# Kernel optimization log

Measured on AMD Instinct MI355X. Metric: run time of the kernel, lower is better.

## Reference

```python
import jax, jax.numpy as jnp
import numpy as np

# ---- static config (from init_kwargs) ----
SAMPLE_RATE = 2048.0
MAX_SHIFT = int(0.025 * SAMPLE_RATE)          # 51 samples
NUM_BINS = 16
FFTLENGTH = 1.0                               # chisq_kernel_length (s)
DF = 1.0 / FFTLENGTH
NUM_FREQS = int(FFTLENGTH * SAMPLE_RATE // 2 + 1)   # 1025 == rfft bins of 2048 samples
HIGHPASS = 32.0
CHISQ_PENALTY = 1.0
_freqs = np.arange(NUM_FREQS) / FFTLENGTH
MASK = _freqs >= HIGHPASS                     # static numpy bool mask

BATCH, CHANNELS, DIM = 256, 2, 2048


def setup_inputs() -> dict:
    key = jax.random.key(0)
    k1, k2 = jax.random.split(key)
    x_hat = jax.random.normal(k1, (BATCH, CHANNELS, DIM), dtype=jnp.float32)
    x = jax.random.normal(k2, (BATCH, CHANNELS, DIM), dtype=jnp.float32)
    return {"x_hat": x_hat, "x": x}


def _center(x):
    xmin = x.min(-1, keepdims=True)
    xmax = x.max(-1, keepdims=True)
    return 2 * (x - xmin) / (xmax - xmin) - 1


def _shifted_pearson(x, y, max_shift):
    # x, y: [B, C, T]; returns corr: [W, B, C] with W = 2*max_shift + 1
    b, c, t = x.shape
    num_windows = 2 * max_shift + 1
    xp = jnp.pad(x, ((0, 0), (0, 0), (max_shift, max_shift)))
    # window w, position i -> xp[..., i + w]  (same layout as torch unfold)
    idx = jnp.arange(num_windows)[:, None] + jnp.arange(t)[None, :]   # [W, T]
    xw = xp[:, :, idx]                                                # [B, C, W, T]
    xw = jnp.transpose(xw, (2, 0, 1, 3))                              # [W, B, C, T]
    xw = xw - xw.mean(-1, keepdims=True)
    yc = y - y.mean(-1, keepdims=True)
    corr = (xw * yc).sum(-1)
    norm = (xw ** 2).sum(-1) * (yc ** 2).sum(-1)
    return corr / jnp.sqrt(norm)


def _snr_integral(a, b):
    # |4 * a * conj(b) * df| cumulatively summed over frequency
    integrand = a * jnp.conj(b)
    return jnp.abs(4 * integrand * DF).cumsum(-1)


def _chisq(htilde, stilde):
    htilde = htilde[:, :, MASK]
    stilde = stilde[:, :, MASK]
    # partition frequencies by the template's own optimal-SNR integral
    si = _snr_integral(htilde, htilde)                    # [B, C, F]
    total = si[:, :, -1:]
    bins = (jnp.arange(NUM_BINS + 1, dtype=si.dtype) / NUM_BINS) * total  # [B, C, NB+1]
    search = jax.vmap(jax.vmap(lambda a, v: jnp.searchsorted(a, v, side="right")))
    edges = search(si, bins)
    edges = jnp.clip(edges, 0, si.shape[-1] - 1)
    qtilde = htilde / jnp.sqrt(total).astype(htilde.dtype)
    # SNR per bin of the normalized template against the strain
    si2 = _snr_integral(qtilde, stilde)                   # [B, C, F]
    total2 = si2[:, :, -1:]
    right = jnp.take_along_axis(si2, edges[:, :, 1:], axis=-1)
    left = jnp.take_along_axis(si2, edges[:, :, :-1], axis=-1)
    snr_per_bin = right - left                            # [B, C, NB]
    summand = (snr_per_bin - total2 / NUM_BINS) ** 2
    chisq = NUM_BINS * summand.sum(-1) / (NUM_BINS - 1)
    return total2[:, :, 0], chisq


def reference(x_hat, x):
    x_hat = _center(x_hat)
    corr = _shifted_pearson(x_hat, x, MAX_SHIFT)          # [W, B, C]
    corr = corr.max(0)                                    # [B, C]
    loss = (1 - corr) / (1 + corr)
    htilde = jnp.fft.rfft(x_hat, axis=-1) / SAMPLE_RATE   # [B, C, 1025] complex
    stilde = jnp.fft.rfft(x, axis=-1) / SAMPLE_RATE
    _, chisq = _chisq(htilde, stilde)
    chisq = chisq * CHISQ_PENALTY
    loss = loss * (1 + chisq ** 3) ** (1.0 / 6.0)
    return loss
```

## Files before the change

kernel.cpp:

```cpp
#include <hip/hip_runtime.h>
#include <math.h>

#define ROWS 512
#define DIM 2048
#define MS 51
#define NWIN 103
#define KMIN 32
#define NMASK 993

__global__ __launch_bounds__(512) void fused_mfl_kernel(
    const float* __restrict__ xhat, const float* __restrict__ x,
    float* __restrict__ out)
{
    const int r = blockIdx.x;
    const int t = threadIdx.x;
    const int lane = t & 63;
    const int wave = t >> 6;

    __shared__ float smem[13056];
    float2* A2  = (float2*)smem;
    float2* B2  = (float2*)(smem + 4096);
    float2* TW  = (float2*)(smem + 8192);
    float2* Qlo = (float2*)smem;
    float2* Qhi = (float2*)smem + 1024;
    float* siA  = smem + 4096;
    float* siBr = smem + 5120;
    float* red6 = smem + 9216;
    float* ah   = smem + 12288;
    float* xhd  = smem + 12339;
    float* at_  = smem + 12390;
    float* xt_  = smem + 12441;
    float* Ah   = smem + 12492;
    float* Aqh  = smem + 12544;
    float* Xh   = smem + 12596;
    float* At   = smem + 12648;
    float* Aqt  = smem + 12700;
    float* Xt   = smem + 12752;
    float* corrv= smem + 12804;
    float* accv = smem + 12907;

    __shared__ float sc[8];
    __shared__ int   edges[17];
    __shared__ float summ[16];
    __shared__ float wsA[4], wsB[4];

    const float* xhp = xhat + (size_t)r * DIM;
    const float* xrp = x    + (size_t)r * DIM;
    float av[4] = {xhp[t], xhp[t+512], xhp[t+1024], xhp[t+1536]};
    float bv[4] = {xrp[t], xrp[t+512], xrp[t+1024], xrp[t+1536]};

    float swv, cwv;
    __sincosf((float)t * (-3.14159265358979323846f / 1024.0f), &swv, &cwv);
    TW[t] = make_float2(cwv, swv);

    {
        float mn4 = fminf(fminf(av[0],av[1]), fminf(av[2],av[3]));
        float mx4 = fmaxf(fmaxf(av[0],av[1]), fmaxf(av[2],av[3]));
        float sa = (av[0]+av[1])+(av[2]+av[3]);
        float qa = (av[0]*av[0]+av[1]*av[1])+(av[2]*av[2]+av[3]*av[3]);
        float sx = (bv[0]+bv[1])+(bv[2]+bv[3]);
        float qx = (bv[0]*bv[0]+bv[1]*bv[1])+(bv[2]*bv[2]+bv[3]*bv[3]);
        red6[t] = mn4; red6[512+t] = mx4; red6[1024+t] = sa;
        red6[1536+t] = qa; red6[2048+t] = sx; red6[2560+t] = qx;
    }
    if (t < MS)   { ah[t] = av[0];      xhd[t] = bv[0]; }
    if (t >= 461) { at_[t-461] = av[3]; xt_[t-461] = bv[3]; }
    {
        float t0r=av[0]+av[2], t0i=bv[0]+bv[2];
        float t1r=av[0]-av[2], t1i=bv[0]-bv[2];
        float t2r=av[1]+av[3], t2i=bv[1]+bv[3];
        float d3r=av[1]-av[3], d3i=bv[1]-bv[3];
        float t3r=d3i, t3i=-d3r;
        float w1r=cwv, w1i=swv;
        float w2r=w1r*w1r-w1i*w1i, w2i=2.f*w1r*w1i;
        float w3r=w2r*w1r-w2i*w1i, w3i=w2r*w1i+w2i*w1r;
        float y0r=t0r+t2r, y0i=t0i+t2i;
        float a1r=t1r+t3r, a1i=t1i+t3i;
        float y1r=a1r*w1r-a1i*w1i, y1i=a1r*w1i+a1i*w1r;
        float a2r=t0r-t2r, a2i=t0i-t2i;
        float y2r=a2r*w2r-a2i*w2i, y2i=a2r*w2i+a2i*w2r;
        float a3r=t1r-t3r, a3i=t1i-t3i;
        float y3r=a3r*w3r-a3i*w3i, y3i=a3r*w3i+a3i*w3r;
        A2[4*t]   = make_float2(y0r,y0i);
        A2[4*t+1] = make_float2(y1r,y1i);
        A2[4*t+2] = make_float2(y2r,y2i);
        A2[4*t+3] = make_float2(y3r,y3i);
    }
    __syncthreads();

    auto fft2048_r8 = [&](const float2* Sp, float2* Dp, const int s, const bool tw) {
        const int q = t;
        const int u = q & ~(s - 1);
        float2 x0=Sp[q],      x1=Sp[q+256],  x2=Sp[q+512],  x3=Sp[q+768];
        float2 x4=Sp[q+1024], x5=Sp[q+1280], x6=Sp[q+1536], x7=Sp[q+1792];
        float e0r=x0.x+x4.x, e0i=x0.y+x4.y;
        float e1r=x0.x-x4.x, e1i=x0.y-x4.y;
        float e2r=x2.x+x6.x, e2i=x2.y+x6.y;
        float e3r=x2.x-x6.x, e3i=x2.y-x6.y;
        float A0r=e0r+e2r, A0i=e0i+e2i;
        float A1r=e1r+e3i, A1i=e1i-e3r;
        float A2r_=e0r-e2r, A2i_=e0i-e2i;
        float A3r=e1r-e3i, A3i=e1i+e3r;
        float o0r=x1.x+x5.x, o0i=x1.y+x5.y;
        float o1r=x1.x-x5.x, o1i=x1.y-x5.y;
        float o2r=x3.x+x7.x, o2i=x3.y+x7.y;
        float o3r=x3.x-x7.x, o3i=x3.y-x7.y;
        float B0r=o0r+o2r, B0i=o0i+o2i;
        float B1r=o1r+o3i, B1i=o1i-o3r;
        float B2r_=o0r-o2r, B2i_=o0i-o2i;
        float B3r=o1r-o3i, B3i=o1i+o3r;
        const float RT = 0.70710678118654752f;
        float C1r = RT*(B1r + B1i), C1i = RT*(B1i - B1r);
        float C2r = B2i_,           C2i = -B2r_;
        float C3r = RT*(B3i - B3r), C3i = -RT*(B3r + B3i);
        float y0r=A0r+B0r,  y0i=A0i+B0i;
        float y1r=A1r+C1r,  y1i=A1i+C1i;
        float y2r=A2r_+C2r, y2i=A2i_+C2i;
        float y3r=A3r+C3r,  y3i=A3i+C3i;
        float y4r=A0r-B0r,  y4i=A0i-B0i;
        float y5r=A1r-C1r,  y5i=A1i-C1i;
        float y6r=A2r_-C2r, y6i=A2i_-C2i;
        float y7r=A3r-C3r,  y7i=A3i-C3i;
        int base = q + 7*u;
        Dp[base] = make_float2(y0r, y0i);
        if (tw) {
            float2 w1 = TW[u];
            auto cm = [](float ar, float ai, float br, float bi, float* rr, float* ri) {
                *rr = ar*br - ai*bi; *ri = ar*bi + ai*br;
            };
            float w2r,w2i,w3r,w3i,w4r,w4i,w5r,w5i,w6r,w6i,w7r,w7i;
            cm(w1.x,w1.y,w1.x,w1.y,&w2r,&w2i);
            cm(w2r,w2i,w1.x,w1.y,&w3r,&w3i);
            cm(w2r,w2i,w2r,w2i,&w4r,&w4i);
            cm(w2r,w2i,w3r,w3i,&w5r,&w5i);
            cm(w3r,w3i,w3r,w3i,&w6r,&w6i);
            cm(w3r,w3i,w4r,w4i,&w7r,&w7i);
            float rr, ri;
            cm(y1r,y1i,w1.x,w1.y,&rr,&ri); Dp[base+s]   = make_float2(rr,ri);
            cm(y2r,y2i,w2r,w2i,&rr,&ri);   Dp[base+2*s] = make_float2(rr,ri);
            cm(y3r,y3i,w3r,w3i,&rr,&ri);   Dp[base+3*s] = make_float2(rr,ri);
            cm(y4r,y4i,w4r,w4i,&rr,&ri);   Dp[base+4*s] = make_float2(rr,ri);
            cm(y5r,y5i,w5r,w5i,&rr,&ri);   Dp[base+5*s] = make_float2(rr,ri);
            cm(y6r,y6i,w6r,w6i,&rr,&ri);   Dp[base+6*s] = make_float2(rr,ri);
            cm(y7r,y7i,w7r,w7i,&rr,&ri);   Dp[base+7*s] = make_float2(rr,ri);
        } else {
            Dp[base+s]   = make_float2(y1r,y1i);
            Dp[base+2*s] = make_float2(y2r,y2i);
            Dp[base+3*s] = make_float2(y3r,y3i);
            Dp[base+4*s] = make_float2(y4r,y4i);
            Dp[base+5*s] = make_float2(y5r,y5i);
            Dp[base+6*s] = make_float2(y6r,y6i);
            Dp[base+7*s] = make_float2(y7r,y7i);
        }
    };
    auto fft1024 = [&](const float2* Sp, float2* Dp, const int s) {
        const int q = t;
        const int u = q & ~(s - 1);
        float2 x0 = Sp[q], x1 = Sp[q+256], x2 = Sp[q+512], x3 = Sp[q+768];
        float t0r=x0.x+x2.x, t0i=x0.y+x2.y;
        float t1r=x0.x-x2.x, t1i=x0.y-x2.y;
        float t2r=x1.x+x3.x, t2i=x1.y+x3.y;
        float d3r=x1.x-x3.x, d3i=x1.y-x3.y;
        float t3r=d3i, t3i=-d3r;
        float2 w1 = TW[2*u];
        float w2r=w1.x*w1.x-w1.y*w1.y, w2i=2.f*w1.x*w1.y;
        float w3r=w2r*w1.x-w2i*w1.y,  w3i=w2r*w1.y+w2i*w1.x;
        float y0r=t0r+t2r, y0i=t0i+t2i;
        float a1r=t1r+t3r, a1i=t1i+t3i;
        float y1r=a1r*w1.x-a1i*w1.y, y1i=a1r*w1.y+a1i*w1.x;
        float a2r=t0r-t2r, a2i=t0i-t2i;
        float y2r=a2r*w2r-a2i*w2i, y2i=a2r*w2i+a2i*w2r;
        float a3r=t1r-t3r, a3i=t1i-t3i;
        float y3r=a3r*w3r-a3i*w3i, y3i=a3r*w3i+a3i*w3r;
        int base = q + 3*u;
        Dp[base]     = make_float2(y0r,y0i);
        Dp[base+s]   = make_float2(y1r,y1i);
        Dp[base+2*s] = make_float2(y2r,y2i);
        Dp[base+3*s] = make_float2(y3r,y3i);
    };

    if (t < 256) {
        fft2048_r8(A2, B2, 4, true);
    } else if (wave == 4) {
        float4 u, v;
        u=((const float4*)(red6     ))[2*lane]; v=((const float4*)(red6     ))[2*lane+1];
        float pmn=fminf(fminf(fminf(u.x,u.y),fminf(u.z,u.w)),fminf(fminf(v.x,v.y),fminf(v.z,v.w)));
        u=((const float4*)(red6+ 512))[2*lane]; v=((const float4*)(red6+ 512))[2*lane+1];
        float pmx=fmaxf(fmaxf(fmaxf(u.x,u.y),fmaxf(u.z,u.w)),fmaxf(fmaxf(v.x,v.y),fmaxf(v.z,v.w)));
        u=((const float4*)(red6+1024))[2*lane]; v=((const float4*)(red6+1024))[2*lane+1];
        float psa=((u.x+u.y)+(u.z+u.w))+((v.x+v.y)+(v.z+v.w));
        u=((const float4*)(red6+1536))[2*lane]; v=((const float4*)(red6+1536))[2*lane+1];
        float pqa=((u.x+u.y)+(u.z+u.w))+((v.x+v.y)+(v.z+v.w));
        u=((const float4*)(red6+2048))[2*lane]; v=((const float4*)(red6+2048))[2*lane+1];
        float psx=((u.x+u.y)+(u.z+u.w))+((v.x+v.y)+(v.z+v.w));
        u=((const float4*)(red6+2560))[2*lane]; v=((const float4*)(red6+2560))[2*lane+1];
        float pqx=((u.x+u.y)+(u.z+u.w))+((v.x+v.y)+(v.z+v.w));
#pragma unroll
        for (int d = 32; d; d >>= 1) {
            pmn=fminf(pmn,__shfl_down(pmn,d)); pmx=fmaxf(pmx,__shfl_down(pmx,d));
            psa+=__shfl_down(psa,d); pqa+=__shfl_down(pqa,d);
            psx+=__shfl_down(psx,d); pqx+=__shfl_down(pqx,d);
        }
        if (lane == 0) {
            float scl = 2.0f/(pmx - pmn);
            float Cc  = scl*pmn + 1.0f;
            float mean = psx * (1.0f/DIM);
            sc[0]=scl; sc[1]=Cc; sc[2]=mean; sc[3]=psa; sc[4]=pqa;
            sc[5]=pqx - (float)DIM*mean*mean;
        }
    } else if (wave == 5) {
        float va=0.f, vq=0.f, vx=0.f;
        if (lane >= 1 && lane <= MS) { float aa=ah[lane-1]; va=aa; vq=aa*aa; vx=xhd[lane-1]; }
#pragma unroll
        for (int d = 1; d < 64; d <<= 1) {
            float ya=__shfl_up(va,d), yq=__shfl_up(vq,d), yx=__shfl_up(vx,d);
            if (lane >= d) { va+=ya; vq+=yq; vx+=yx; }
        }
        if (lane <= MS) { Ah[lane]=va; Aqh[lane]=vq; Xh[lane]=vx; }
    } else if (wave == 6) {
        float va=0.f, vq=0.f, vx=0.f;
        if (lane >= 1 && lane <= MS) { float aa=at_[MS-lane]; va=aa; vq=aa*aa; vx=xt_[MS-lane]; }
#pragma unroll
        for (int d = 1; d < 64; d <<= 1) {
            float ya=__shfl_up(va,d), yq=__shfl_up(vq,d), yx=__shfl_up(vx,d);
            if (lane >= d) { va+=ya; vq+=yq; vx+=yx; }
        }
        if (lane <= MS) { At[lane]=va; Aqt[lane]=vq; Xt[lane]=vx; }
    }
    __syncthreads();
    if (t < 256) { fft2048_r8(B2, A2, 32, true); }
    __syncthreads();
    if (t < 256) { fft2048_r8(A2, B2, 256, false); }
    __syncthreads();

    const float scl = sc[0], Cc = sc[1], mean = sc[2];
    const float Sa = sc[3], Qa = sc[4], Szz = sc[5];
    const float MSC = 0.5f * (1.0f / 2048.0f);

    float se0=0,se1=0,se2=0,se3=0, sg0=0,sg1=0,sg2=0,sg3=0;
    float incE=0, incG=0, totE=0, totG=0;

    if (t < 256) {
        const int q = t;
        float2 wA = TW[q], wB = TW[q + 256];
        auto mkQ = [&](int k, float2 w, int ni) -> float2 {
            float2 Pa, Pb;
            if (k == 0) {
                float2 Xm = B2[1024];
                Pa = make_float2(0.f, 0.f);
                Pb = make_float2(4.f * Xm.x * Xm.y, 0.f);
            } else {
                float2 Xk = B2[k], Xn = B2[2048-k];
                float hre = Xk.x + Xn.x, him = Xk.y - Xn.y;
                float sre = Xk.y + Xn.y, sim = Xn.x - Xk.x;
                Pa = make_float2(hre*sre + him*sim, -(him*sre - hre*sim));
                float2 Xm = B2[1024-k], Xp = B2[1024+k];
                float hre2 = Xm.x + Xp.x, him2 = Xm.y - Xp.y;
                float sre2 = Xm.y + Xp.y, sim2 = Xp.x - Xm.x;
                Pb = make_float2(hre2*sre2 + him2*sim2, him2*sre2 - hre2*sim2);
            }
            float D1r = Pa.x + Pb.x, D1i = Pa.y + Pb.y;
            float D2r = Pa.x - Pb.x, D2i = Pa.y - Pb.y;
            float Er = D2r*w.x - D2i*w.y;
            float Ei = D2r*w.y + D2i*w.x;
            if (ni) return make_float2(D1r - Er, D1i - Ei);
            return make_float2(D1r + Ei, D1i - Er);
        };
        float2 x0 = mkQ(q,     wA, 0);
        float2 x1 = mkQ(q+256, wB, 0);
        float2 x2 = mkQ(q+512, wA, 1);
        float2 x3 = mkQ(q+768, wB, 1);
        float t0r=x0.x+x2.x, t0i=x0.y+x2.y;
        float t1r=x0.x-x2.x, t1i=x0.y-x2.y;
        float t2r=x1.x+x3.x, t2i=x1.y+x3.y;
        float d3r=x1.x-x3.x, d3i=x1.y-x3.y;
        float t3r=d3i, t3i=-d3r;
        float2 w1 = TW[2*q];
        float w2r=w1.x*w1.x-w1.y*w1.y, w2i=2.f*w1.x*w1.y;
        float w3r=w2r*w1.x-w2i*w1.y,  w3i=w2r*w1.y+w2i*w1.x;
        float y0r=t0r+t2r, y0i=t0i+t2i;
        float a1r=t1r+t3r, a1i=t1i+t3i;
        float y1r=a1r*w1.x-a1i*w1.y, y1i=a1r*w1.y+a1i*w1.x;
        float a2r=t0r-t2r, a2i=t0i-t2i;
        float y2r=a2r*w2r-a2i*w2i, y2i=a2r*w2i+a2i*w2r;
        float a3r=t1r-t3r, a3i=t1i-t3i;
        float y3r=a3r*w3r-a3i*w3i, y3i=a3r*w3i+a3i*w3r;
        Qlo[4*q]   = make_float2(y0r,y0i);
        Qlo[4*q+1] = make_float2(y1r,y1i);
        Qlo[4*q+2] = make_float2(y2r,y2i);
        Qlo[4*q+3] = make_float2(y3r,y3i);
    } else {
        int tt = t - 256;
        float ee[4], gg[4];
#pragma unroll
        for (int j = 0; j < 4; ++j) {
            int m = 4*tt + j;
            ee[j] = 0.f; gg[j] = 0.f;
            if (m < NMASK) {
                int f = m + KMIN;
                float2 Xf = B2[f], Xg = B2[2048-f];
                float hre = Xf.x + Xg.x, him = Xf.y - Xg.y;
                float sre = Xf.y + Xg.y, sim = Xg.x - Xf.x;
                float hm = scl * sqrtf(hre*hre + him*him) * MSC;
                float sm = sqrtf(sre*sre + sim*sim) * MSC;
                ee[j] = 4.f*hm*hm; gg[j] = 4.f*hm*sm;
            }
        }
        se0=ee[0]; se1=se0+ee[1]; se2=se1+ee[2]; se3=se2+ee[3];
        sg0=gg[0]; sg1=sg0+gg[1]; sg2=sg1+gg[2]; sg3=sg2+gg[3];
        totE=se3; totG=sg3; incE=totE; incG=totG;
#pragma unroll
        for (int d = 1; d < 64; d <<= 1) {
            float yE=__shfl_up(incE,d), yG=__shfl_up(incG,d);
            if (lane >= d) { incE+=yE; incG+=yG; }
        }
        if (lane == 63) { wsA[wave-4]=incE; wsB[wave-4]=incG; }
    }
    __syncthreads();

    if (t < 256) { fft1024(Qlo, Qhi, 4); }
    else {
        int tt = t - 256, w4 = wave - 4;
        float offE=0.f, offG=0.f;
        for (int w = 0; w < w4; ++w) { offE+=wsA[w]; offG+=wsB[w]; }
        float preE = offE + incE - totE;
        float preG = offG + incG - totG;
        ((float4*)siA)[tt]  = make_float4(preE+se0, preE+se1, preE+se2, preE+se3);
        ((float4*)siBr)[tt] = make_float4(preG+sg0, preG+sg1, preG+sg2, preG+sg3);
    }
    __syncthreads();

    if (t < 256) { fft1024(Qhi, Qlo, 16); }
    else if (t < 256 + 17) {
        int tl = t - 256;
        float total = siA[NMASK-1];
        float bin = ((float)tl * (1.0f/16.0f)) * total;
        int lo = 0, hi = NMASK;
        while (lo < hi) { int mid=(lo+hi)>>1; if (siA[mid] <= bin) lo=mid+1; else hi=mid; }
        edges[tl] = (lo < NMASK-1) ? lo : (NMASK-1);
    }
    __syncthreads();

    if (t < 256) { fft1024(Qlo, Qhi, 64); }
    else {
        int idx = t - 256;
        if (idx < 16) {
            float total = siA[NMASK-1];
            float qf = 1.0f / sqrtf(total);
            float total2 = siBr[NMASK-1] * qf;
            float snr = (siBr[edges[idx+1]] - siBr[edges[idx]]) * qf;
            float d = snr - total2 * (1.0f/16.0f);
            summ[idx] = d * d;
        }
        int c = idx >> 1, k2 = idx & 1;
        if (c < NWIN) {
            int off = c - MS;
            float acc = 0.f;
            if (off > 0) {
                for (int j = k2; j < off; j += 2) acc += ah[j] * (xt_[MS-off+j] - mean);
            } else if (off < 0) {
                int o = -off;
                for (int j = k2; j < o; j += 2) acc += at_[MS-o+j] * (xhd[j] - mean);
            }
            acc += __shfl_down(acc, 1);
            if (k2 == 0) accv[c] = acc;
        }
    }
    __syncthreads();

    if (t < NWIN) {
        int c = t;
        int off = c - MS;
        int sidx = (off >= 0) ? off : (2048 + off);
        int n = sidx >> 1;
        int q = n & 255;
        float2 x0 = Qhi[q], x1 = Qhi[q+256], x2 = Qhi[q+512], x3 = Qhi[q+768];
        float2 Fv;
        if (n < 256) {
            Fv = make_float2((x0.x+x2.x)+(x1.x+x3.x), (x0.y+x2.y)+(x1.y+x3.y));
        } else {
            float t1r_ = x0.x - x2.x, t1i_ = x0.y - x2.y;
            float d3r_ = x1.x - x3.x, d3i_ = x1.y - x3.y;
            Fv = make_float2(t1r_ - d3i_, t1i_ + d3r_);
        }
        float val = (sidx & 1) ? -Fv.y : Fv.x;
        float circ = val * (1.0f/8192.0f);
        float acc = accv[c];
        float Sin_a, Sin_q, Zex, nin;
        if (off >= 0) {
            Sin_a = Sa - Ah[off]; Sin_q = Qa - Aqh[off];
            Zex = Xt[off] - (float)off * mean; nin = 2048.0f - (float)off;
        } else {
            int o = -off;
            Sin_a = Sa - At[o]; Sin_q = Qa - Aqt[o];
            Zex = Xh[o] - (float)o * mean; nin = 2048.0f - (float)o;
        }
        float num = scl * (circ - acc) + Cc * Zex;
        float Sw  = scl * Sin_a - Cc * nin;
        float Sw2 = scl*scl*Sin_q - 2.f*scl*Cc*Sin_a + Cc*Cc*nin;
        float varw = Sw2 - Sw * Sw * (1.0f/2048.0f);
        corrv[c] = num / sqrtf(varw * Szz);
    }
    __syncthreads();

    if (wave == 0) {
        float m = corrv[lane];
        if (lane + 64 < NWIN) m = fmaxf(m, corrv[lane + 64]);
#pragma unroll
        for (int d = 32; d; d >>= 1) m = fmaxf(m, __shfl_down(m, d));
        if (lane == 0) {
            float loss0 = (1.0f - m) / (1.0f + m);
            float ss = 0.f;
            for (int i = 0; i < 16; ++i) ss += summ[i];
            float chisq = 16.0f * ss / 15.0f;
            float c3 = chisq * chisq * chisq;
            out[r] = loss0 * __powf(1.0f + c3, 1.0f/6.0f);
        }
    }
}

extern "C" void kernel_launch(void* const* d_in, const int* in_sizes, int n_in,
                              void* d_out, int out_size, void* d_ws, size_t ws_size,
                              hipStream_t stream) {
    const float* xhat = (const float*)d_in[0];
    const float* x    = (const float*)d_in[1];
    float* out = (float*)d_out;
    (void)in_sizes; (void)n_in; (void)out_size; (void)d_ws; (void)ws_size;

    fused_mfl_kernel<<<ROWS, 512, 0, stream>>>(xhat, x, out);
}
```

Measured before the change: 65.75 us.

## Use radix-8 FFT for 1024-point stages and merge tail phases to cut barriers

Replaces the three radix-4 passes of the 1024-point FFT with two radix-8 passes run by 128 threads, which removes one barrier-separated phase. The accv computation moves earlier so it runs alongside the 2048-point FFT. The chi-square edge search and bin reduction are folded into a single wave using shuffles, and the correlation evaluation is fused with its max reduction in wave 0. Together these drop several __syncthreads and shared-memory round trips, at the cost of fewer active threads during the 1024-point FFT passes.

New measurement: 66.57 us. Within noise of the previous version (+1.2%).

```diff
diff --git a/kernel.cpp b/kernel.cpp
--- a/kernel.cpp
+++ b/kernel.cpp
@@ -36,12 +36,9 @@
     float* At   = smem + 12648;
     float* Aqt  = smem + 12700;
     float* Xt   = smem + 12752;
-    float* corrv= smem + 12804;
-    float* accv = smem + 12907;
+    float* accv = smem + 12804;
 
     __shared__ float sc[8];
-    __shared__ int   edges[17];
-    __shared__ float summ[16];
     __shared__ float wsA[4], wsB[4];
 
     const float* xhp = xhat + (size_t)r * DIM;
@@ -88,11 +85,12 @@
     }
     __syncthreads();
 
-    auto fft2048_r8 = [&](const float2* Sp, float2* Dp, const int s, const bool tw) {
+    auto fft_r8 = [&](const float2* Sp, float2* Dp, const int s,
+                      const int rs, const int tm, const bool tw) {
         const int q = t;
         const int u = q & ~(s - 1);
-        float2 x0=Sp[q],      x1=Sp[q+256],  x2=Sp[q+512],  x3=Sp[q+768];
-        float2 x4=Sp[q+1024], x5=Sp[q+1280], x6=Sp[q+1536], x7=Sp[q+1792];
+        float2 x0=Sp[q],      x1=Sp[q+rs],   x2=Sp[q+2*rs], x3=Sp[q+3*rs];
+        float2 x4=Sp[q+4*rs], x5=Sp[q+5*rs], x6=Sp[q+6*rs], x7=Sp[q+7*rs];
         float e0r=x0.x+x4.x, e0i=x0.y+x4.y;
         float e1r=x0.x-x4.x, e1i=x0.y-x4.y;
         float e2r=x2.x+x6.x, e2i=x2.y+x6.y;
@@ -124,7 +122,7 @@
         int base = q + 7*u;
         Dp[base] = make_float2(y0r, y0i);
         if (tw) {
-            float2 w1 = TW[u];
+            float2 w1 = TW[tm*u];
             auto cm = [](float ar, float ai, float br, float bi, float* rr, float* ri) {
                 *rr = ar*br - ai*bi; *ri = ar*bi + ai*br;
             };
@@ -153,34 +151,9 @@
             Dp[base+7*s] = make_float2(y7r,y7i);
         }
     };
-    auto fft1024 = [&](const float2* Sp, float2* Dp, const int s) {
-        const int q = t;
-        const int u = q & ~(s - 1);
-        float2 x0 = Sp[q], x1 = Sp[q+256], x2 = Sp[q+512], x3 = Sp[q+768];
-        float t0r=x0.x+x2.x, t0i=x0.y+x2.y;
-        float t1r=x0.x-x2.x, t1i=x0.y-x2.y;
-        float t2r=x1.x+x3.x, t2i=x1.y+x3.y;
-        float d3r=x1.x-x3.x, d3i=x1.y-x3.y;
-        float t3r=d3i, t3i=-d3r;
-        float2 w1 = TW[2*u];
-        float w2r=w1.x*w1.x-w1.y*w1.y, w2i=2.f*w1.x*w1.y;
-        float w3r=w2r*w1.x-w2i*w1.y,  w3i=w2r*w1.y+w2i*w1.x;
-        float y0r=t0r+t2r, y0i=t0i+t2i;
-        float a1r=t1r+t3r, a1i=t1i+t3i;
-        float y1r=a1r*w1.x-a1i*w1.y, y1i=a1r*w1.y+a1i*w1.x;
-        float a2r=t0r-t2r, a2i=t0i-t2i;
-        float y2r=a2r*w2r-a2i*w2i, y2i=a2r*w2i+a2i*w2r;
-        float a3r=t1r-t3r, a3i=t1i-t3i;
-        float y3r=a3r*w3r-a3i*w3i, y3i=a3r*w3i+a3i*w3r;
-        int base = q + 3*u;
-        Dp[base]     = make_float2(y0r,y0i);
-        Dp[base+s]   = make_float2(y1r,y1i);
-        Dp[base+2*s] = make_float2(y2r,y2i);
-        Dp[base+3*s] = make_float2(y3r,y3i);
-    };
 
     if (t < 256) {
-        fft2048_r8(A2, B2, 4, true);
+        fft_r8(A2, B2, 4, 256, 1, true);
     } else if (wave == 4) {
         float4 u, v;
         u=((const float4*)(red6     ))[2*lane]; v=((const float4*)(red6     ))[2*lane+1];
@@ -228,13 +201,30 @@
         if (lane <= MS) { At[lane]=va; Aqt[lane]=vq; Xt[lane]=vx; }
     }
     __syncthreads();
-    if (t < 256) { fft2048_r8(B2, A2, 32, true); }
-    __syncthreads();
-    if (t < 256) { fft2048_r8(A2, B2, 256, false); }
-    __syncthreads();
-
-    const float scl = sc[0], Cc = sc[1], mean = sc[2];
-    const float Sa = sc[3], Qa = sc[4], Szz = sc[5];
+
+    if (t < 256) {
+        fft_r8(B2, A2, 32, 256, 1, true);
+    } else {
+        int idx = t - 256;
+        int c = idx >> 1, k2 = idx & 1;
+        if (c < NWIN) {
+            const float mean = sc[2];
+            int off = c - MS;
+            float acc = 0.f;
+            if (off > 0) {
+                for (int j = k2; j < off; j += 2) acc += ah[j] * (xt_[MS-off+j] - mean);
+            } else if (off < 0) {
+                int o = -off;
+                for (int j = k2; j < o; j += 2) acc += at_[MS-o+j] * (xhd[j] - mean);
+            }
+            acc += __shfl_down(acc, 1);
+            if (k2 == 0) accv[c] = acc;
+        }
+    }
+    __syncthreads();
+    if (t < 256) { fft_r8(A2, B2, 256, 256, 1, false); }
+    __syncthreads();
+
     const float MSC = 0.5f * (1.0f / 2048.0f);
 
     float se0=0,se1=0,se2=0,se3=0, sg0=0,sg1=0,sg2=0,sg3=0;
@@ -290,6 +280,7 @@
         Qlo[4*q+2] = make_float2(y2r,y2i);
         Qlo[4*q+3] = make_float2(y3r,y3i);
     } else {
+        const float scl = sc[0];
         int tt = t - 256;
         float ee[4], gg[4];
 #pragma unroll
@@ -318,8 +309,9 @@
     }
     __syncthreads();
 
-    if (t < 256) { fft1024(Qlo, Qhi, 4); }
-    else {
+    if (t < 128) {
+        fft_r8(Qlo, Qhi, 4, 128, 2, true);
+    } else if (t >= 256) {
         int tt = t - 256, w4 = wave - 4;
         float offE=0.f, offG=0.f;
         for (int w = 0; w < w4; ++w) { offE+=wsA[w]; offG+=wsB[w]; }
@@ -330,91 +322,83 @@
     }
     __syncthreads();
 
-    if (t < 256) { fft1024(Qhi, Qlo, 16); }
-    else if (t < 256 + 17) {
-        int tl = t - 256;
+    if (t < 128) {
+        fft_r8(Qhi, Qlo, 32, 128, 2, true);
+    } else if (wave == 4) {
         float total = siA[NMASK-1];
-        float bin = ((float)tl * (1.0f/16.0f)) * total;
-        int lo = 0, hi = NMASK;
-        while (lo < hi) { int mid=(lo+hi)>>1; if (siA[mid] <= bin) lo=mid+1; else hi=mid; }
-        edges[tl] = (lo < NMASK-1) ? lo : (NMASK-1);
-    }
-    __syncthreads();
-
-    if (t < 256) { fft1024(Qlo, Qhi, 64); }
-    else {
-        int idx = t - 256;
-        if (idx < 16) {
-            float total = siA[NMASK-1];
-            float qf = 1.0f / sqrtf(total);
-            float total2 = siBr[NMASK-1] * qf;
-            float snr = (siBr[edges[idx+1]] - siBr[edges[idx]]) * qf;
+        float qf = 1.0f / sqrtf(total);
+        float total2 = siBr[NMASK-1] * qf;
+        int lo = NMASK - 1;
+        if (lane < 17) {
+            float bin = ((float)lane * (1.0f/16.0f)) * total;
+            int l0 = 0, hi = NMASK;
+            while (l0 < hi) { int mid=(l0+hi)>>1; if (siA[mid] <= bin) l0=mid+1; else hi=mid; }
+            lo = (l0 < NMASK-1) ? l0 : (NMASK-1);
+        }
+        int lon = __shfl_down(lo, 1);
+        float sv = 0.f;
+        if (lane < 16) {
+            float snr = (siBr[lon] - siBr[lo]) * qf;
             float d = snr - total2 * (1.0f/16.0f);
-            summ[idx] = d * d;
-        }
-        int c = idx >> 1, k2 = idx & 1;
-        if (c < NWIN) {
-            int off = c - MS;
-            float acc = 0.f;
-            if (off > 0) {
-                for (int j = k2; j < off; j += 2) acc += ah[j] * (xt_[MS-off+j] - mean);
-            } else if (off < 0) {
-                int o = -off;
-                for (int j = k2; j < o; j += 2) acc += at_[MS-o+j] * (xhd[j] - mean);
+            sv = d * d;
+        }
+        sv += __shfl_down(sv, 8);
+        sv += __shfl_down(sv, 4);
+        sv += __shfl_down(sv, 2);
+        sv += __shfl_down(sv, 1);
+        if (lane == 0) {
+            float chisq = 16.0f * sv / 15.0f;
+            float c3 = chisq * chisq * chisq;
+            sc[7] = __powf(1.0f + c3, 1.0f/6.0f);
+        }
+    }
+    __syncthreads();
+
+    if (wave == 0) {
+        const float scl = sc[0], Cc = sc[1], mean = sc[2];
+        const float Sa = sc[3], Qa = sc[4], Szz = sc[5];
+        float m = -2.0f;
+#pragma unroll
+        for (int rep = 0; rep < 2; ++rep) {
+            int c = lane + 64 * rep;
+            if (c < NWIN) {
+                int off = c - MS;
+                int sidx = (off >= 0) ? off : (2048 + off);
+                int n = sidx >> 1;
+                int q = n & 255;
+                float2 x0 = Qlo[q], x1 = Qlo[q+256], x2 = Qlo[q+512], x3 = Qlo[q+768];
+                float2 Fv;
+                if (n < 256) {
+                    Fv = make_float2((x0.x+x2.x)+(x1.x+x3.x), (x0.y+x2.y)+(x1.y+x3.y));
+                } else {
+                    float t1r_ = x0.x - x2.x, t1i_ = x0.y - x2.y;
+                    float d3r_ = x1.x - x3.x, d3i_ = x1.y - x3.y;
+                    Fv = make_float2(t1r_ - d3i_, t1i_ + d3r_);
+                }
+                float val = (sidx & 1) ? -Fv.y : Fv.x;
+                float circ = val * (1.0f/8192.0f);
+                float acc = accv[c];
+                float Sin_a, Sin_q, Zex, nin;
+                if (off >= 0) {
+                    Sin_a = Sa - Ah[off]; Sin_q = Qa - Aqh[off];
+                    Zex = Xt[off] - (float)off * mean; nin = 2048.0f - (float)off;
+                } else {
+                    int o = -off;
+                    Sin_a = Sa - At[o]; Sin_q = Qa - Aqt[o];
+                    Zex = Xh[o] - (float)o * mean; nin = 2048.0f - (float)o;
+                }
+                float num = scl * (circ - acc) + Cc * Zex;
+                float Sw  = scl * Sin_a - Cc * nin;
+                float Sw2 = scl*scl*Sin_q - 2.f*scl*Cc*Sin_a + Cc*Cc*nin;
+                float varw = Sw2 - Sw * Sw * (1.0f/2048.0f);
+                m = fmaxf(m, num / sqrtf(varw * Szz));
             }
-            acc += __shfl_down(acc, 1);
-            if (k2 == 0) accv[c] = acc;
-        }
-    }
-    __syncthreads();
-
-    if (t < NWIN) {
-        int c = t;
-        int off = c - MS;
-        int sidx = (off >= 0) ? off : (2048 + off);
-        int n = sidx >> 1;
-        int q = n & 255;
-        float2 x0 = Qhi[q], x1 = Qhi[q+256], x2 = Qhi[q+512], x3 = Qhi[q+768];
-        float2 Fv;
-        if (n < 256) {
-            Fv = make_float2((x0.x+x2.x)+(x1.x+x3.x), (x0.y+x2.y)+(x1.y+x3.y));
-        } else {
-            float t1r_ = x0.x - x2.x, t1i_ = x0.y - x2.y;
-            float d3r_ = x1.x - x3.x, d3i_ = x1.y - x3.y;
-            Fv = make_float2(t1r_ - d3i_, t1i_ + d3r_);
-        }
-        float val = (sidx & 1) ? -Fv.y : Fv.x;
-        float circ = val * (1.0f/8192.0f);
-        float acc = accv[c];
-        float Sin_a, Sin_q, Zex, nin;
-        if (off >= 0) {
-            Sin_a = Sa - Ah[off]; Sin_q = Qa - Aqh[off];
-            Zex = Xt[off] - (float)off * mean; nin = 2048.0f - (float)off;
-        } else {
-            int o = -off;
-            Sin_a = Sa - At[o]; Sin_q = Qa - Aqt[o];
-            Zex = Xh[o] - (float)o * mean; nin = 2048.0f - (float)o;
-        }
-        float num = scl * (circ - acc) + Cc * Zex;
-        float Sw  = scl * Sin_a - Cc * nin;
-        float Sw2 = scl*scl*Sin_q - 2.f*scl*Cc*Sin_a + Cc*Cc*nin;
-        float varw = Sw2 - Sw * Sw * (1.0f/2048.0f);
-        corrv[c] = num / sqrtf(varw * Szz);
-    }
-    __syncthreads();
-
-    if (wave == 0) {
-        float m = corrv[lane];
-        if (lane + 64 < NWIN) m = fmaxf(m, corrv[lane + 64]);
+        }
 #pragma unroll
         for (int d = 32; d; d >>= 1) m = fmaxf(m, __shfl_down(m, d));
         if (lane == 0) {
             float loss0 = (1.0f - m) / (1.0f + m);
-            float ss = 0.f;
-            for (int i = 0; i < 16; ++i) ss += summ[i];
-            float chisq = 16.0f * ss / 15.0f;
-            float c3 = chisq * chisq * chisq;
-            out[r] = loss0 * __powf(1.0f + c3, 1.0f/6.0f);
+            out[r] = loss0 * sc[7];
         }
     }
 }
```
